# Performance work log

Measured on AMD Instinct MI355X. Metric: run time of the kernel, lower is better.

## Reference

```python
import jax, jax.numpy as jnp
import numpy as np

D_MODEL = 1024
N_HEADS = 16
HEAD_DIM = D_MODEL // N_HEADS
B, S = 2, 2048


def setup_inputs() -> dict:
    key = jax.random.key(0)
    ks = jax.random.split(key, 12)
    std = 1.0 / np.sqrt(D_MODEL)
    mk = lambda k: (jax.random.normal(k, (D_MODEL, D_MODEL), jnp.float32) * std)
    return {
        "query": jax.random.normal(ks[0], (B, S, D_MODEL), jnp.float32),
        "key": jax.random.normal(ks[1], (B, S, D_MODEL), jnp.float32),
        "value": jax.random.normal(ks[2], (B, S, D_MODEL), jnp.float32),
        "Wq": mk(ks[3]), "bq": jnp.zeros((D_MODEL,), jnp.float32),
        "Wk": mk(ks[4]), "bk": jnp.zeros((D_MODEL,), jnp.float32),
        "Wv": mk(ks[5]), "bv": jnp.zeros((D_MODEL,), jnp.float32),
        "Wo": mk(ks[6]), "bo": jnp.zeros((D_MODEL,), jnp.float32),
    }


def reference(query, key, value, Wq, bq, Wk, bk, Wv, bv, Wo, bo):
    b, s, d = query.shape
    # Linear projections (torch Linear: x @ W.T + b)
    q = query @ Wq.T + bq
    k = key @ Wk.T + bk
    v = value @ Wv.T + bv
    # [B, H, S, Dh]
    split = lambda x: x.reshape(b, -1, N_HEADS, HEAD_DIM).transpose(0, 2, 1, 3)
    qh, kh, vh = split(q), split(k), split(v)
    scores = jnp.einsum("bhqd,bhkd->bhqk", qh, kh) / jnp.sqrt(
        jnp.asarray(HEAD_DIM, qh.dtype))
    attn = jax.nn.softmax(scores, axis=-1)
    out = jnp.einsum("bhqk,bhkd->bhqd", attn, vh)
    out = out.transpose(0, 2, 1, 3).reshape(b, -1, N_HEADS * HEAD_DIM)
    return out @ Wo.T + bo
```

## Files before the change

kernel.cpp:

```cpp
#include <hip/hip_runtime.h>
#include <hip/hip_bf16.h>


typedef short bf16x8 __attribute__((ext_vector_type(8)));
typedef short bf16x4 __attribute__((ext_vector_type(4)));
typedef float f32x4  __attribute__((ext_vector_type(4)));

constexpr size_t NE = (size_t)4096 * 1024;
constexpr size_t NW = (size_t)1024 * 1024;

#if __has_builtin(__builtin_amdgcn_exp2f)
#define EXP2(x) __builtin_amdgcn_exp2f(x)
#else
#define EXP2(x) exp2f(x)
#endif

__device__ __forceinline__ short f2bf(float f) {
  __hip_bfloat16 h = __float2bfloat16(f);
  return *reinterpret_cast<short*>(&h);
}

__device__ __forceinline__ void cp16(const short* g, short* l) {
  __builtin_amdgcn_global_load_lds(
      (const __attribute__((address_space(1))) void*)g,
      (__attribute__((address_space(3))) void*)l, 16, 0, 0);
}

__global__ __launch_bounds__(256) void cvt_kernel(
    const float* q, const float* k, const float* v,
    const float* Wq, const float* Wk, const float* Wv, const float* Wo,
    short* qb, short* kb, short* vb,
    short* Wqb, short* Wkb, short* Wvb, short* Wob) {
  const int y = blockIdx.y;
  const float* s; short* d;
  if (y < 12) {
    const int t = y >> 2;
    const size_t off = (size_t)(y & 3) << 20;
    s = (t == 0 ? q : (t == 1 ? k : v)) + off;
    d = (t == 0 ? qb : (t == 1 ? kb : vb)) + off;
  } else {
    s = (y == 12 ? Wq : (y == 13 ? Wk : (y == 14 ? Wv : Wo)));
    d = (y == 12 ? Wqb : (y == 13 ? Wkb : (y == 14 ? Wvb : Wob)));
  }
  size_t i = (size_t)blockIdx.x * 256 + threadIdx.x;
  float4 val = ((const float4*)s)[i];
  bf16x4 o;
  o[0] = f2bf(val.x); o[1] = f2bf(val.y); o[2] = f2bf(val.z); o[3] = f2bf(val.w);
  ((bf16x4*)d)[i] = o;
}

__global__ __launch_bounds__(256) void gemm_qkv(
    const short* __restrict__ A0, const short* __restrict__ A1, const short* __restrict__ A2,
    const short* __restrict__ W0, const short* __restrict__ W1, const short* __restrict__ W2,
    const float* __restrict__ b0, const float* __restrict__ b1, const float* __restrict__ b2,
    short* __restrict__ C0, short* __restrict__ C1, short* __restrict__ Cv) {
  __shared__ short As[2][128 * 32];
  __shared__ short Bs[2][128 * 32];
  const int which = blockIdx.y;
  const short* A    = which == 0 ? A0 : (which == 1 ? A1 : A2);
  const short* W    = which == 0 ? W0 : (which == 1 ? W1 : W2);
  const float* bias = which == 0 ? b0 : (which == 1 ? b1 : b2);
  const float scale = which == 0 ? 0.18033688011112042f : 1.0f;

  const int tid  = threadIdx.x;
  const int bm   = (int)blockIdx.x >> 3;
  const int bn   = (int)blockIdx.x & 7;
  const int lane = tid & 63, wid = tid >> 6;
  const int g = lane >> 4, l15 = lane & 15;
  const int wm = (wid >> 1) * 64, wn = (wid & 1) * 64;

  const short* Ag = A + (size_t)(bm * 128 + (tid >> 2)) * 1024 + (tid & 3) * 8;
  const short* Wg = W + (size_t)(bn * 128 + (tid >> 2)) * 1024 + (tid & 3) * 8;
  const int wofs = wid * 512;

  f32x4 acc[4][4];
#pragma unroll
  for (int i = 0; i < 4; ++i)
#pragma unroll
    for (int j = 0; j < 4; ++j) acc[i][j] = (f32x4){0.f, 0.f, 0.f, 0.f};

  for (int k0 = 0; k0 < 1024; k0 += 64) {
    __syncthreads();
#pragma unroll
    for (int p = 0; p < 2; ++p) {
      const int kk = k0 + p * 32;
      cp16(Ag + kk,             As[p] + wofs);
      cp16(Ag + 64 * 1024 + kk, As[p] + wofs + 2048);
      cp16(Wg + kk,             Bs[p] + wofs);
      cp16(Wg + 64 * 1024 + kk, Bs[p] + wofs + 2048);
    }
    __syncthreads();

#pragma unroll
    for (int p = 0; p < 2; ++p) {
      bf16x8 af[4], bf[4];
#pragma unroll
      for (int mt = 0; mt < 4; ++mt)
        af[mt] = *(const bf16x8*)&As[p][(wm + mt * 16 + l15) * 32 + g * 8];
#pragma unroll
      for (int nt = 0; nt < 4; ++nt)
        bf[nt] = *(const bf16x8*)&Bs[p][(wn + nt * 16 + l15) * 32 + g * 8];
#pragma unroll
      for (int mt = 0; mt < 4; ++mt)
#pragma unroll
        for (int nt = 0; nt < 4; ++nt)
          acc[mt][nt] = __builtin_amdgcn_mfma_f32_16x16x32_bf16(
              af[mt], bf[nt], acc[mt][nt], 0, 0, 0);
    }
  }

  const int col0 = bn * 128 + wn;
  if (which < 2) {
    short* C = which == 0 ? C0 : C1;
#pragma unroll
    for (int nt = 0; nt < 4; ++nt) {
      const int col = col0 + nt * 16 + l15;
      const float bb = bias[col];
#pragma unroll
      for (int mt = 0; mt < 4; ++mt) {
        const int m0 = bm * 128 + wm + mt * 16 + g * 4;
#pragma unroll
        for (int r = 0; r < 4; ++r)
          C[(size_t)(m0 + r) * 1024 + col] = f2bf((acc[mt][nt][r] + bb) * scale);
      }
    }
  } else {
#pragma unroll
    for (int nt = 0; nt < 4; ++nt) {
      const int col = col0 + nt * 16 + l15;
      const int h = col >> 6, dh = col & 63;
      const float bb = bias[col];
#pragma unroll
      for (int mt = 0; mt < 4; ++mt) {
        const int m0 = bm * 128 + wm + mt * 16 + g * 4;
        const int bb_ = m0 >> 11, s0 = m0 & 2047;
        bf16x4 o;
#pragma unroll
        for (int r = 0; r < 4; ++r) o[r] = f2bf(acc[mt][nt][r] + bb);
        *(bf16x4*)&Cv[(((size_t)bb_ * 16 + h) * 64 + dh) * 2048 + s0] = o;
      }
    }
  }
}

__global__ __launch_bounds__(256) void gemm_out(
    const short* __restrict__ A, const short* __restrict__ W,
    const float* __restrict__ bias, float* __restrict__ C) {
  __shared__ short As[2][64 * 32];
  __shared__ short Bs[2][128 * 32];
  const int tid  = threadIdx.x;
  const int bm   = (int)blockIdx.x >> 3;
  const int bn   = (int)blockIdx.x & 7;
  const int lane = tid & 63, wid = tid >> 6;
  const int g = lane >> 4, l15 = lane & 15;
  const int wm = (wid >> 1) * 32, wn = (wid & 1) * 64;

  const short* Ag = A + (size_t)(bm * 64 + (tid >> 2)) * 1024 + (tid & 3) * 8;
  const short* Wg = W + (size_t)(bn * 128 + (tid >> 2)) * 1024 + (tid & 3) * 8;
  const int wofs = wid * 512;

  f32x4 acc[2][4];
#pragma unroll
  for (int i = 0; i < 2; ++i)
#pragma unroll
    for (int j = 0; j < 4; ++j) acc[i][j] = (f32x4){0.f, 0.f, 0.f, 0.f};

  for (int k0 = 0; k0 < 1024; k0 += 64) {
    __syncthreads();
#pragma unroll
    for (int p = 0; p < 2; ++p) {
      const int kk = k0 + p * 32;
      cp16(Ag + kk,             As[p] + tid * 8 - tid * 8 + wofs);
      cp16(Wg + kk,             Bs[p] + wofs);
      cp16(Wg + 64 * 1024 + kk, Bs[p] + wofs + 2048);
    }
    __syncthreads();

#pragma unroll
    for (int p = 0; p < 2; ++p) {
      bf16x8 af[2], bf[4];
#pragma unroll
      for (int mt = 0; mt < 2; ++mt)
        af[mt] = *(const bf16x8*)&As[p][(wm + mt * 16 + l15) * 32 + g * 8];
#pragma unroll
      for (int nt = 0; nt < 4; ++nt)
        bf[nt] = *(const bf16x8*)&Bs[p][(wn + nt * 16 + l15) * 32 + g * 8];
#pragma unroll
      for (int mt = 0; mt < 2; ++mt)
#pragma unroll
        for (int nt = 0; nt < 4; ++nt)
          acc[mt][nt] = __builtin_amdgcn_mfma_f32_16x16x32_bf16(
              af[mt], bf[nt], acc[mt][nt], 0, 0, 0);
    }
  }

  const int col0 = bn * 128 + wn;
#pragma unroll
  for (int nt = 0; nt < 4; ++nt) {
    const int col = col0 + nt * 16 + l15;
    const float bb = bias[col];
#pragma unroll
    for (int mt = 0; mt < 2; ++mt) {
      const int m0 = bm * 64 + wm + mt * 16 + g * 4;
#pragma unroll
      for (int r = 0; r < 4; ++r)
        C[(size_t)(m0 + r) * 1024 + col] = acc[mt][nt][r] + bb;
    }
  }
}

__global__ __launch_bounds__(256) void attn_kernel(
    const short* __restrict__ Q, const short* __restrict__ K,
    const short* __restrict__ Vg, short* __restrict__ O) {
  __shared__ short Kt[64][72];
  __shared__ short Vt[64][72];
  __shared__ short Pt[4][32][72];

  const int tid  = threadIdx.x;
  const int qt   = (int)blockIdx.x & 15;
  const int bh   = (int)blockIdx.x >> 4;
  const int b    = bh >> 4, h = bh & 15;
  const int lane = tid & 63, wid = tid >> 6;
  const int g = lane >> 4, l15 = lane & 15;

  const int q0 = qt * 128 + wid * 32;
  bf16x8 qf[2][2];
#pragma unroll
  for (int mt = 0; mt < 2; ++mt) {
    const size_t base = (size_t)(b * 2048 + q0 + mt * 16 + l15) * 1024 + h * 64;
    qf[mt][0] = *(const bf16x8*)(Q + base + g * 8);
    qf[mt][1] = *(const bf16x8*)(Q + base + 32 + g * 8);
  }

  f32x4 o_acc[2][4];
#pragma unroll
  for (int i = 0; i < 2; ++i)
#pragma unroll
    for (int j = 0; j < 4; ++j) o_acc[i][j] = (f32x4){0.f, 0.f, 0.f, 0.f};
  float l_i[2][4];
#pragma unroll
  for (int i = 0; i < 2; ++i)
#pragma unroll
    for (int r = 0; r < 4; ++r) l_i[i][r] = 0.f;

  const int srow = tid >> 2, sch = tid & 3;
  const short* Kbase = K + (size_t)(b * 2048) * 1024 + h * 64 + sch * 8;
  const short* Vbase = Vg + (size_t)((b * 16 + h) * 64 + srow) * 2048 + sch * 8;

  bf16x8 nk0, nk1, nv0, nv1;
  {
    const short* krow = Kbase + (size_t)srow * 1024;
    nk0 = *(const bf16x8*)(krow);
    nk1 = *(const bf16x8*)(krow + 32);
    nv0 = *(const bf16x8*)(Vbase);
    nv1 = *(const bf16x8*)(Vbase + 32);
  }

  for (int kt = 0; kt < 32; ++kt) {
    __syncthreads();
    *(bf16x8*)&Kt[srow][sch * 8]      = nk0;
    *(bf16x8*)&Kt[srow][sch * 8 + 32] = nk1;
    *(bf16x8*)&Vt[srow][sch * 8]      = nv0;
    *(bf16x8*)&Vt[srow][sch * 8 + 32] = nv1;
    __syncthreads();

    if (kt < 31) {
      const short* krow = Kbase + (size_t)((kt + 1) * 64 + srow) * 1024;
      nk0 = *(const bf16x8*)(krow);
      nk1 = *(const bf16x8*)(krow + 32);
      nv0 = *(const bf16x8*)(Vbase + (kt + 1) * 64);
      nv1 = *(const bf16x8*)(Vbase + (kt + 1) * 64 + 32);
    }

    f32x4 sv[2][4];
#pragma unroll
    for (int nt = 0; nt < 4; ++nt) {
      bf16x8 kf0 = *(const bf16x8*)&Kt[nt * 16 + l15][g * 8];
      bf16x8 kf1 = *(const bf16x8*)&Kt[nt * 16 + l15][32 + g * 8];
#pragma unroll
      for (int mt = 0; mt < 2; ++mt) {
        f32x4 z = (f32x4){0.f, 0.f, 0.f, 0.f};
        z = __builtin_amdgcn_mfma_f32_16x16x32_bf16(qf[mt][0], kf0, z, 0, 0, 0);
        z = __builtin_amdgcn_mfma_f32_16x16x32_bf16(qf[mt][1], kf1, z, 0, 0, 0);
        sv[mt][nt] = z;
      }
    }

#pragma unroll
    for (int mt = 0; mt < 2; ++mt)
#pragma unroll
      for (int r = 0; r < 4; ++r) {
        float p0 = EXP2(sv[mt][0][r]);
        float p1 = EXP2(sv[mt][1][r]);
        float p2 = EXP2(sv[mt][2][r]);
        float p3 = EXP2(sv[mt][3][r]);
        l_i[mt][r] += (p0 + p1) + (p2 + p3);
        const int pr = mt * 16 + g * 4 + r;
        Pt[wid][pr][l15]      = f2bf(p0);
        Pt[wid][pr][16 + l15] = f2bf(p1);
        Pt[wid][pr][32 + l15] = f2bf(p2);
        Pt[wid][pr][48 + l15] = f2bf(p3);
      }

    bf16x8 pf[2][2];
#pragma unroll
    for (int mt = 0; mt < 2; ++mt) {
      pf[mt][0] = *(const bf16x8*)&Pt[wid][mt * 16 + l15][g * 8];
      pf[mt][1] = *(const bf16x8*)&Pt[wid][mt * 16 + l15][32 + g * 8];
    }
#pragma unroll
    for (int nt = 0; nt < 4; ++nt) {
      bf16x8 vf0 = *(const bf16x8*)&Vt[nt * 16 + l15][g * 8];
      bf16x8 vf1 = *(const bf16x8*)&Vt[nt * 16 + l15][32 + g * 8];
#pragma unroll
      for (int mt = 0; mt < 2; ++mt) {
        o_acc[mt][nt] = __builtin_amdgcn_mfma_f32_16x16x32_bf16(
            pf[mt][0], vf0, o_acc[mt][nt], 0, 0, 0);
        o_acc[mt][nt] = __builtin_amdgcn_mfma_f32_16x16x32_bf16(
            pf[mt][1], vf1, o_acc[mt][nt], 0, 0, 0);
      }
    }
  }

#pragma unroll
  for (int mt = 0; mt < 2; ++mt)
#pragma unroll
    for (int r = 0; r < 4; ++r) {
      float l = l_i[mt][r];
#pragma unroll
      for (int off = 1; off < 16; off <<= 1) l += __shfl_xor(l, off, 64);
      const float inv = 1.0f / l;
      const int row = q0 + mt * 16 + g * 4 + r;
      const size_t base = (size_t)(b * 2048 + row) * 1024 + h * 64;
#pragma unroll
      for (int nt = 0; nt < 4; ++nt)
        O[base + nt * 16 + l15] = f2bf(o_acc[mt][nt][r] * inv);
    }
}

extern "C" void kernel_launch(void* const* d_in, const int* in_sizes, int n_in,
                              void* d_out, int out_size, void* d_ws, size_t ws_size,
                              hipStream_t stream) {
  (void)in_sizes; (void)n_in; (void)out_size; (void)ws_size;
  const float* q  = (const float*)d_in[0];
  const float* k  = (const float*)d_in[1];
  const float* v  = (const float*)d_in[2];
  const float* Wq = (const float*)d_in[3];
  const float* bq = (const float*)d_in[4];
  const float* Wk = (const float*)d_in[5];
  const float* bk = (const float*)d_in[6];
  const float* Wv = (const float*)d_in[7];
  const float* bv = (const float*)d_in[8];
  const float* Wo = (const float*)d_in[9];
  const float* bo = (const float*)d_in[10];
  float* out = (float*)d_out;

  short* qb  = (short*)d_ws;
  short* kb  = qb + NE;
  short* vb  = kb + NE;
  short* Wqb = vb + NE;
  short* Wkb = Wqb + NW;
  short* Wvb = Wkb + NW;
  short* Wob = Wvb + NW;
  short* Qw  = Wob + NW;
  short* Kw  = Qw + NE;
  short* Vtg = Kw + NE;
  short* Ob  = qb;

  cvt_kernel<<<dim3(1024, 16), 256, 0, stream>>>(q, k, v, Wq, Wk, Wv, Wo,
                                                 qb, kb, vb, Wqb, Wkb, Wvb, Wob);
  gemm_qkv<<<dim3(256, 3), 256, 0, stream>>>(qb, kb, vb, Wqb, Wkb, Wvb,
                                             bq, bk, bv, Qw, Kw, Vtg);
  attn_kernel<<<512, 256, 0, stream>>>(Qw, Kw, Vtg, Ob);
  gemm_out<<<512, 256, 0, stream>>>(Ob, Wob, bo, out);
}
```

Measured before the change: 240.7 us.

## Split attention key loop across two wave groups with LDS reduction

Doubles the attention block to 512 threads, with two groups of four waves processing alternating 64-key tiles so each group runs half as many iterations. Partial output accumulators and row sums from the second group are written to shared memory and added into the first group before normalization. This aims to raise wave-level parallelism and hide latency on the serial KV loop, at the cost of more LDS per block and an extra reduction step.

Result: faster. 230.8 us (-4.1%).

```diff
diff --git a/kernel.cpp b/kernel.cpp
--- a/kernel.cpp
+++ b/kernel.cpp
@@ -170,7 +170,7 @@
 #pragma unroll
     for (int p = 0; p < 2; ++p) {
       const int kk = k0 + p * 32;
-      cp16(Ag + kk,             As[p] + tid * 8 - tid * 8 + wofs);
+      cp16(Ag + kk,             As[p] + wofs);
       cp16(Wg + kk,             Bs[p] + wofs);
       cp16(Wg + 64 * 1024 + kk, Bs[p] + wofs + 2048);
     }
@@ -209,21 +209,25 @@
   }
 }
 
-__global__ __launch_bounds__(256) void attn_kernel(
+__global__ __launch_bounds__(512) void attn_kernel(
     const short* __restrict__ Q, const short* __restrict__ K,
     const short* __restrict__ Vg, short* __restrict__ O) {
-  __shared__ short Kt[64][72];
-  __shared__ short Vt[64][72];
-  __shared__ short Pt[4][32][72];
+  __shared__ __align__(16) char smem[73728];
+  short (*Kt)[64][72] = (short(*)[64][72])smem;
+  short (*Vt)[64][72] = (short(*)[64][72])(smem + 18432);
+  short (*Pt)[32][72] = (short(*)[32][72])(smem + 36864);
+  float* M = (float*)smem;
 
   const int tid  = threadIdx.x;
   const int qt   = (int)blockIdx.x & 15;
   const int bh   = (int)blockIdx.x >> 4;
   const int b    = bh >> 4, h = bh & 15;
   const int lane = tid & 63, wid = tid >> 6;
+  const int par  = wid >> 2;
+  const int w4   = wid & 3;
   const int g = lane >> 4, l15 = lane & 15;
 
-  const int q0 = qt * 128 + wid * 32;
+  const int q0 = qt * 128 + w4 * 32;
   bf16x8 qf[2][2];
 #pragma unroll
   for (int mt = 0; mt < 2; ++mt) {
@@ -243,40 +247,43 @@
 #pragma unroll
     for (int r = 0; r < 4; ++r) l_i[i][r] = 0.f;
 
-  const int srow = tid >> 2, sch = tid & 3;
+  const int st   = tid & 255;
+  const int spar = tid >> 8;
+  const int srow = st >> 2, sch = st & 3;
   const short* Kbase = K + (size_t)(b * 2048) * 1024 + h * 64 + sch * 8;
   const short* Vbase = Vg + (size_t)((b * 16 + h) * 64 + srow) * 2048 + sch * 8;
 
   bf16x8 nk0, nk1, nv0, nv1;
   {
-    const short* krow = Kbase + (size_t)srow * 1024;
+    const short* krow = Kbase + (size_t)(spar * 64 + srow) * 1024;
     nk0 = *(const bf16x8*)(krow);
     nk1 = *(const bf16x8*)(krow + 32);
-    nv0 = *(const bf16x8*)(Vbase);
-    nv1 = *(const bf16x8*)(Vbase + 32);
-  }
-
-  for (int kt = 0; kt < 32; ++kt) {
-    __syncthreads();
-    *(bf16x8*)&Kt[srow][sch * 8]      = nk0;
-    *(bf16x8*)&Kt[srow][sch * 8 + 32] = nk1;
-    *(bf16x8*)&Vt[srow][sch * 8]      = nv0;
-    *(bf16x8*)&Vt[srow][sch * 8 + 32] = nv1;
-    __syncthreads();
-
-    if (kt < 31) {
-      const short* krow = Kbase + (size_t)((kt + 1) * 64 + srow) * 1024;
+    nv0 = *(const bf16x8*)(Vbase + spar * 64);
+    nv1 = *(const bf16x8*)(Vbase + spar * 64 + 32);
+  }
+
+  for (int ktp = 0; ktp < 16; ++ktp) {
+    __syncthreads();
+    *(bf16x8*)&Kt[spar][srow][sch * 8]      = nk0;
+    *(bf16x8*)&Kt[spar][srow][sch * 8 + 32] = nk1;
+    *(bf16x8*)&Vt[spar][srow][sch * 8]      = nv0;
+    *(bf16x8*)&Vt[spar][srow][sch * 8 + 32] = nv1;
+    __syncthreads();
+
+    if (ktp < 15) {
+      const int kn = (ktp + 1) * 2 + spar;
+      const short* krow = Kbase + (size_t)(kn * 64 + srow) * 1024;
       nk0 = *(const bf16x8*)(krow);
       nk1 = *(const bf16x8*)(krow + 32);
-      nv0 = *(const bf16x8*)(Vbase + (kt + 1) * 64);
-      nv1 = *(const bf16x8*)(Vbase + (kt + 1) * 64 + 32);
+      nv0 = *(const bf16x8*)(Vbase + kn * 64);
+      nv1 = *(const bf16x8*)(Vbase + kn * 64 + 32);
     }
 
     f32x4 sv[2][4];
 #pragma unroll
     for (int nt = 0; nt < 4; ++nt) {
-      bf16x8 kf0 = *(const bf16x8*)&Kt[nt * 16 + l15][g * 8];
-      bf16x8 kf1 = *(const bf16x8*)&Kt[nt * 16 + l15][32 + g * 8];
+      bf16x8 kf0 = *(const bf16x8*)&Kt[par][nt * 16 + l15][g * 8];
+      bf16x8 kf1 = *(const bf16x8*)&Kt[par][nt * 16 + l15][32 + g * 8];
 #pragma unroll
       for (int mt = 0; mt < 2; ++mt) {
         f32x4 z = (f32x4){0.f, 0.f, 0.f, 0.f};
@@ -310,8 +317,8 @@
     }
 #pragma unroll
     for (int nt = 0; nt < 4; ++nt) {
-      bf16x8 vf0 = *(const bf16x8*)&Vt[nt * 16 + l15][g * 8];
-      bf16x8 vf1 = *(const bf16x8*)&Vt[nt * 16 + l15][32 + g * 8];
+      bf16x8 vf0 = *(const bf16x8*)&Vt[par][nt * 16 + l15][g * 8];
+      bf16x8 vf1 = *(const bf16x8*)&Vt[par][nt * 16 + l15][32 + g * 8];
 #pragma unroll
       for (int mt = 0; mt < 2; ++mt) {
         o_acc[mt][nt] = __builtin_amdgcn_mfma_f32_16x16x32_bf16(
@@ -322,20 +329,47 @@
     }
   }
 
-#pragma unroll
-  for (int mt = 0; mt < 2; ++mt)
-#pragma unroll
-    for (int r = 0; r < 4; ++r) {
-      float l = l_i[mt][r];
-#pragma unroll
-      for (int off = 1; off < 16; off <<= 1) l += __shfl_xor(l, off, 64);
-      const float inv = 1.0f / l;
-      const int row = q0 + mt * 16 + g * 4 + r;
-      const size_t base = (size_t)(b * 2048 + row) * 1024 + h * 64;
+  __syncthreads();
+  if (par == 1) {
+    float* dst = M + (size_t)(w4 * 64 + lane) * 40;
+#pragma unroll
+    for (int mt = 0; mt < 2; ++mt)
 #pragma unroll
       for (int nt = 0; nt < 4; ++nt)
-        O[base + nt * 16 + l15] = f2bf(o_acc[mt][nt][r] * inv);
-    }
+        *(f32x4*)(dst + (mt * 4 + nt) * 4) = o_acc[mt][nt];
+#pragma unroll
+    for (int mt = 0; mt < 2; ++mt)
+#pragma unroll
+      for (int r = 0; r < 4; ++r) dst[32 + mt * 4 + r] = l_i[mt][r];
+  }
+  __syncthreads();
+  if (par == 0) {
+    const float* src = M + (size_t)(w4 * 64 + lane) * 40;
+#pragma unroll
+    for (int mt = 0; mt < 2; ++mt)
+#pragma unroll
+      for (int nt = 0; nt < 4; ++nt)
+        o_acc[mt][nt] += *(const f32x4*)(src + (mt * 4 + nt) * 4);
+#pragma unroll
+    for (int mt = 0; mt < 2; ++mt)
+#pragma unroll
+      for (int r = 0; r < 4; ++r) l_i[mt][r] += src[32 + mt * 4 + r];
+
+#pragma unroll
+    for (int mt = 0; mt < 2; ++mt)
+#pragma unroll
+      for (int r = 0; r < 4; ++r) {
+        float l = l_i[mt][r];
+#pragma unroll
+        for (int off = 1; off < 16; off <<= 1) l += __shfl_xor(l, off, 64);
+        const float inv = 1.0f / l;
+        const int row = q0 + mt * 16 + g * 4 + r;
+        const size_t base = (size_t)(b * 2048 + row) * 1024 + h * 64;
+#pragma unroll
+        for (int nt = 0; nt < 4; ++nt)
+          O[base + nt * 16 + l15] = f2bf(o_acc[mt][nt][r] * inv);
+      }
+  }
 }
 
 extern "C" void kernel_launch(void* const* d_in, const int* in_sizes, int n_in,
@@ -371,6 +405,6 @@
                                                  qb, kb, vb, Wqb, Wkb, Wvb, Wob);
   gemm_qkv<<<dim3(256, 3), 256, 0, stream>>>(qb, kb, vb, Wqb, Wkb, Wvb,
                                              bq, bk, bv, Qw, Kw, Vtg);
-  attn_kernel<<<512, 256, 0, stream>>>(Qw, Kw, Vtg, Ob);
+  attn_kernel<<<512, 512, 0, stream>>>(Qw, Kw, Vtg, Ob);
   gemm_out<<<512, 256, 0, stream>>>(Ob, Wob, bo, out);
 }
```
